# Performance work log

Hardware: AMD Instinct MI355X
Metric: run time of the kernel (lower is better)

Reference implementation:

```python
import jax, jax.numpy as jnp
import numpy as np

N_BINS = 10  # module default n_bins


def setup_inputs() -> dict:
    key = jax.random.key(0)
    k1, k2 = jax.random.split(key)
    N, C = 1_000_000, 64
    logits = jax.random.normal(k1, (N, C), dtype=jnp.float32)
    labels = jax.random.randint(k2, (N,), 0, C)
    return {"logits": logits, "labels": labels, "train": 1}


def _ece_from_conf(confidences, correctness, n_bins):
    # bin i covers (i/n_bins, (i+1)/n_bins]; conf > 1/C > 0 after softmax so
    # ceil(conf*n_bins)-1 reproduces the gt(lower)*le(upper) masking.
    bin_idx = jnp.clip(jnp.ceil(confidences * n_bins).astype(jnp.int32) - 1, 0, n_bins - 1)
    ones = jnp.ones_like(confidences)
    counts = jax.ops.segment_sum(ones, bin_idx, num_segments=n_bins)
    conf_sum = jax.ops.segment_sum(confidences, bin_idx, num_segments=n_bins)
    corr_sum = jax.ops.segment_sum(correctness.astype(confidences.dtype), bin_idx, num_segments=n_bins)
    n_total = confidences.shape[0]
    safe = jnp.maximum(counts, 1.0)
    per_bin = jnp.abs(conf_sum / safe - corr_sum / safe) * (counts / n_total)
    ece = jnp.sum(jnp.where(counts > 0, per_bin, 0.0))
    return ece.reshape(1)


def reference(logits, labels, train):
    # train is a static Python int, so this branch resolves at trace time.
    if train:
        softmaxes = jax.nn.softmax(logits, axis=1)
        confidences = jnp.max(softmaxes, axis=1)
        predictions = jnp.argmax(softmaxes, axis=1)
    else:
        softmaxes = jax.nn.softmax(logits, axis=0)
        predictions = jnp.argmax(softmaxes, axis=0)
        t = 1e-05  # smooth-max over classes via tempered logsumexp
        confidences = t * jax.scipy.special.logsumexp(softmaxes / t, axis=0)
    correctness = predictions == labels
    return _ece_from_conf(confidences, correctness, N_BINS)
```

## Files before the change

kernel.cpp:

```cpp
#include <hip/hip_runtime.h>
#include <hip/hip_bf16.h>


#define N_BINS 10
#define C 64

#define WS_COUNTER_OFF 30

__global__ void ece_init_ws(double* ws) {
    int t = threadIdx.x;
    if (t < 3 * N_BINS) ws[t] = 0.0;
    if (t == 0) *(unsigned int*)(ws + WS_COUNTER_OFF) = 0u;
}

__global__ __launch_bounds__(256) void ece_main(const float* __restrict__ logits,
                                                const int* __restrict__ labels,
                                                double* __restrict__ gbins,
                                                float* __restrict__ out,
                                                int N) {
    __shared__ float s_cnt[N_BINS];
    __shared__ float s_conf[N_BINS];
    __shared__ float s_corr[N_BINS];
    __shared__ int s_last;
    const int tid = threadIdx.x;
    if (tid < N_BINS) {
        s_cnt[tid] = 0.0f;
        s_conf[tid] = 0.0f;
        s_corr[tid] = 0.0f;
    }
    __syncthreads();

    const int gtid = blockIdx.x * blockDim.x + tid;
    const int gstride = gridDim.x * blockDim.x;

    for (int row = gtid; row < N; row += gstride) {
        const float4* rp = reinterpret_cast<const float4*>(logits + (size_t)row * C);
        const int lbl = labels[row];

        float4 q[16];
        #pragma unroll
        for (int j = 0; j < 16; ++j) q[j] = rp[j];

        float mx = q[0].x, my = q[0].y, mz = q[0].z, mw = q[0].w;
        int ix = 0, iy = 0, iz = 0, iw = 0;
        #pragma unroll
        for (int j = 1; j < 16; ++j) {
            if (q[j].x > mx) { mx = q[j].x; ix = j; }
            if (q[j].y > my) { my = q[j].y; iy = j; }
            if (q[j].z > mz) { mz = q[j].z; iz = j; }
            if (q[j].w > mw) { mw = q[j].w; iw = j; }
        }
        float m = mx; int idx = (ix << 2);
        int cand = (iy << 2) | 1;
        if (my > m || (my == m && cand < idx)) { m = my; idx = cand; }
        cand = (iz << 2) | 2;
        if (mz > m || (mz == m && cand < idx)) { m = mz; idx = cand; }
        cand = (iw << 2) | 3;
        if (mw > m || (mw == m && cand < idx)) { m = mw; idx = cand; }

        float sx = 0.0f, sy = 0.0f, sz = 0.0f, sw = 0.0f;
        #pragma unroll
        for (int j = 0; j < 16; ++j) {
            sx += __expf(q[j].x - m);
            sy += __expf(q[j].y - m);
            sz += __expf(q[j].z - m);
            sw += __expf(q[j].w - m);
        }
        const float conf = 1.0f / ((sx + sy) + (sz + sw));

        int bin = min(max((int)ceilf(conf * (float)N_BINS) - 1, 0), N_BINS - 1);
        atomicAdd(&s_cnt[bin], 1.0f);
        atomicAdd(&s_conf[bin], conf);
        if (idx == lbl) atomicAdd(&s_corr[bin], 1.0f);
    }
    __syncthreads();
    if (tid < N_BINS) {
        if (s_cnt[tid] != 0.0f) {
            atomicAdd(&gbins[tid], (double)s_cnt[tid]);
            atomicAdd(&gbins[N_BINS + tid], (double)s_conf[tid]);
            atomicAdd(&gbins[2 * N_BINS + tid], (double)s_corr[tid]);
        }
    }

    if (tid == 0) {
        __threadfence();
        unsigned int old = atomicAdd((unsigned int*)(gbins + WS_COUNTER_OFF), 1u);
        s_last = (old == gridDim.x - 1) ? 1 : 0;
    }
    __syncthreads();
    if (s_last && tid == 0) {
        __threadfence();
        double ece = 0.0;
        for (int b = 0; b < N_BINS; ++b) {
            double cnt = atomicAdd(&gbins[b], 0.0);
            if (cnt > 0.0) {
                double conf = atomicAdd(&gbins[N_BINS + b], 0.0) / cnt;
                double corr = atomicAdd(&gbins[2 * N_BINS + b], 0.0) / cnt;
                double d = conf - corr;
                if (d < 0.0) d = -d;
                ece += d * (cnt / (double)N);
            }
        }
        out[0] = (float)ece;
    }
}

extern "C" void kernel_launch(void* const* d_in, const int* in_sizes, int n_in,
                              void* d_out, int out_size, void* d_ws, size_t ws_size,
                              hipStream_t stream) {
    const float* logits = (const float*)d_in[0];
    const int* labels = (const int*)d_in[1];
    float* out = (float*)d_out;
    double* gbins = (double*)d_ws;

    const int N = in_sizes[1];

    ece_init_ws<<<1, 64, 0, stream>>>(gbins);
    ece_main<<<2048, 256, 0, stream>>>(logits, labels, gbins, out, N);
}
```

Measured before the change: 451.3 us.

## Stage row tiles through swizzled LDS for coalesced global loads

Each wavefront now loads a 64-row tile with fully coalesced float4 loads, where consecutive lanes read consecutive 16-byte chunks. It writes the tile into XOR-swizzled shared memory and reads it back so each lane holds one full row. This replaces the earlier strided per-thread row loads, which scattered each wave's accesses across memory. The grid shrinks to 512 blocks, 64 KB of LDS per block limits occupancy, and a tail path handles leftover rows.

```diff
diff --git a/kernel.cpp b/kernel.cpp
--- a/kernel.cpp
+++ b/kernel.cpp
@@ -13,11 +13,41 @@
     if (t == 0) *(unsigned int*)(ws + WS_COUNTER_OFF) = 0u;
 }
 
+__device__ __forceinline__ void reduce_row(const float4* q, float& conf, int& idx) {
+    float mx = q[0].x, my = q[0].y, mz = q[0].z, mw = q[0].w;
+    int ix = 0, iy = 0, iz = 0, iw = 0;
+    #pragma unroll
+    for (int j = 1; j < 16; ++j) {
+        if (q[j].x > mx) { mx = q[j].x; ix = j; }
+        if (q[j].y > my) { my = q[j].y; iy = j; }
+        if (q[j].z > mz) { mz = q[j].z; iz = j; }
+        if (q[j].w > mw) { mw = q[j].w; iw = j; }
+    }
+    float m = mx; idx = (ix << 2);
+    int cand = (iy << 2) | 1;
+    if (my > m || (my == m && cand < idx)) { m = my; idx = cand; }
+    cand = (iz << 2) | 2;
+    if (mz > m || (mz == m && cand < idx)) { m = mz; idx = cand; }
+    cand = (iw << 2) | 3;
+    if (mw > m || (mw == m && cand < idx)) { m = mw; idx = cand; }
+
+    float sx = 0.0f, sy = 0.0f, sz = 0.0f, sw = 0.0f;
+    #pragma unroll
+    for (int j = 0; j < 16; ++j) {
+        sx += __expf(q[j].x - m);
+        sy += __expf(q[j].y - m);
+        sz += __expf(q[j].z - m);
+        sw += __expf(q[j].w - m);
+    }
+    conf = 1.0f / ((sx + sy) + (sz + sw));
+}
+
 __global__ __launch_bounds__(256) void ece_main(const float* __restrict__ logits,
                                                 const int* __restrict__ labels,
                                                 double* __restrict__ gbins,
                                                 float* __restrict__ out,
                                                 int N) {
+    __shared__ float s_tile[4][4096];
     __shared__ float s_cnt[N_BINS];
     __shared__ float s_conf[N_BINS];
     __shared__ float s_corr[N_BINS];
@@ -30,49 +60,64 @@
     }
     __syncthreads();
 
-    const int gtid = blockIdx.x * blockDim.x + tid;
-    const int gstride = gridDim.x * blockDim.x;
+    const int lane = tid & 63;
+    const int wid = tid >> 6;
+    const int gw = blockIdx.x * 4 + wid;
+    const int nw = gridDim.x * 4;
+    const int ntiles = N >> 6;
 
-    for (int row = gtid; row < N; row += gstride) {
-        const float4* rp = reinterpret_cast<const float4*>(logits + (size_t)row * C);
-        const int lbl = labels[row];
+    char* tb = (char*)&s_tile[wid][0];
+
+    for (int t = gw; t < ntiles; t += nw) {
+        const char* src = (const char*)logits + (size_t)t * 16384;
 
         float4 q[16];
         #pragma unroll
-        for (int j = 0; j < 16; ++j) q[j] = rp[j];
+        for (int k = 0; k < 16; ++k)
+            q[k] = *(const float4*)(src + k * 1024 + lane * 16);
 
-        float mx = q[0].x, my = q[0].y, mz = q[0].z, mw = q[0].w;
-        int ix = 0, iy = 0, iz = 0, iw = 0;
         #pragma unroll
-        for (int j = 1; j < 16; ++j) {
-            if (q[j].x > mx) { mx = q[j].x; ix = j; }
-            if (q[j].y > my) { my = q[j].y; iy = j; }
-            if (q[j].z > mz) { mz = q[j].z; iz = j; }
-            if (q[j].w > mw) { mw = q[j].w; iw = j; }
+        for (int k = 0; k < 16; ++k) {
+            const int o = k * 1024 + lane * 16;
+            const int dst = o ^ (((o >> 8) & 15) << 4);
+            *(float4*)(tb + dst) = q[k];
         }
-        float m = mx; int idx = (ix << 2);
-        int cand = (iy << 2) | 1;
-        if (my > m || (my == m && cand < idx)) { m = my; idx = cand; }
-        cand = (iz << 2) | 2;
-        if (mz > m || (mz == m && cand < idx)) { m = mz; idx = cand; }
-        cand = (iw << 2) | 3;
-        if (mw > m || (mw == m && cand < idx)) { m = mw; idx = cand; }
+        asm volatile("s_waitcnt lgkmcnt(0)" ::: "memory");
 
-        float sx = 0.0f, sy = 0.0f, sz = 0.0f, sw = 0.0f;
+        float4 r[16];
+        const int rbase = lane << 8;
+        const int rx = (lane & 15) << 4;
         #pragma unroll
-        for (int j = 0; j < 16; ++j) {
-            sx += __expf(q[j].x - m);
-            sy += __expf(q[j].y - m);
-            sz += __expf(q[j].z - m);
-            sw += __expf(q[j].w - m);
-        }
-        const float conf = 1.0f / ((sx + sy) + (sz + sw));
+        for (int j = 0; j < 16; ++j)
+            r[j] = *(const float4*)(tb + (rbase + ((j << 4) ^ rx)));
 
+        float conf; int idx;
+        reduce_row(r, conf, idx);
+
+        const int lbl = labels[t * 64 + lane];
         int bin = min(max((int)ceilf(conf * (float)N_BINS) - 1, 0), N_BINS - 1);
         atomicAdd(&s_cnt[bin], 1.0f);
         atomicAdd(&s_conf[bin], conf);
         if (idx == lbl) atomicAdd(&s_corr[bin], 1.0f);
     }
+
+    if (gw == 0) {
+        const int rem = N & 63;
+        if (lane < rem) {
+            const int row = (N & ~63) + lane;
+            const float4* rp = (const float4*)(logits + (size_t)row * C);
+            float4 r[16];
+            #pragma unroll
+            for (int j = 0; j < 16; ++j) r[j] = rp[j];
+            float conf; int idx;
+            reduce_row(r, conf, idx);
+            int bin = min(max((int)ceilf(conf * (float)N_BINS) - 1, 0), N_BINS - 1);
+            atomicAdd(&s_cnt[bin], 1.0f);
+            atomicAdd(&s_conf[bin], conf);
+            if (idx == labels[row]) atomicAdd(&s_corr[bin], 1.0f);
+        }
+    }
+
     __syncthreads();
     if (tid < N_BINS) {
         if (s_cnt[tid] != 0.0f) {
@@ -116,5 +161,5 @@
     const int N = in_sizes[1];
 
     ece_init_ws<<<1, 64, 0, stream>>>(gbins);
-    ece_main<<<2048, 256, 0, stream>>>(logits, labels, gbins, out, N);
+    ece_main<<<512, 256, 0, stream>>>(logits, labels, gbins, out, N);
 }
```

Result: faster. 372.8 us (-17.4%).
